# Kernel optimization log

Measured on AMD Instinct MI355X. Metric: run time of the kernel, lower is better.

The kernel has to match this reference:

```python
import jax, jax.numpy as jnp
import numpy as np

B, D, N, MH, MV = 4, 1024, 2048, 1024, 1024

def setup_inputs() -> dict:
    key = jax.random.key(0)
    k1, k2, k3, k4, k5 = jax.random.split(key, 5)
    return {
        "x": jax.random.normal(k1, (B, D, N), dtype=jnp.float32),
        "W_Q": jax.random.normal(k2, (MH, D), dtype=jnp.float32),
        "W_K": jax.random.normal(k3, (MH, D), dtype=jnp.float32),
        "W_V": jax.random.normal(k4, (MV, D), dtype=jnp.float32),
        "W_O": jax.random.normal(k5, (D, MV), dtype=jnp.float32),
    }

def reference(x, W_Q, W_K, W_V, W_O):
    # x: [b, d, n] (feature-major). Projections: [b, m, n]
    q = jnp.einsum('hd,bdn->bhn', W_Q, x)
    k = jnp.einsum('hd,bdn->bhn', W_K, x)
    v = jnp.einsum('vd,bdn->bvn', W_V, x)
    # scores[b,i,j] = sum_h k[b,h,i] * q[b,h,j]  -> [b, n, n]; NOTE: no 1/sqrt scale (faithful)
    scores = jnp.einsum('bhi,bhj->bij', k, q)
    scores = jax.nn.softmax(scores, axis=-1)
    # v @ scores -> [b, m_V, n]
    attn = jnp.einsum('bvi,bij->bvj', v, scores)
    # W_O @ attn -> [b, d, n]
    return jnp.einsum('dv,bvj->bdj', W_O, attn)
```

## Files before the change

kernel.cpp:

```cpp
#include <hip/hip_runtime.h>
#include <cstddef>
#include <cstdint>

typedef unsigned short u16;
typedef __attribute__((ext_vector_type(8))) short bf16x8;
typedef __attribute__((ext_vector_type(8))) _Float16 f16x8;
typedef __attribute__((ext_vector_type(4))) float f32x4;
typedef __attribute__((ext_vector_type(16))) float f32x16;

#define GLOBAL_AS __attribute__((address_space(1)))
#define LDS_AS __attribute__((address_space(3)))

__device__ __forceinline__ void async16(const u16* g, u16* l) {
    __builtin_amdgcn_global_load_lds((GLOBAL_AS const uint32_t*)g,
                                     (LDS_AS uint32_t*)l, 16, 0, 0);
}

__device__ __forceinline__ u16 f2bf(float f) {
    uint32_t u = __builtin_bit_cast(uint32_t, f);
    uint32_t r = (u + 0x7FFFu + ((u >> 16) & 1u)) >> 16;
    return (u16)r;
}

__global__ __launch_bounds__(256)
void wprep(const float* __restrict__ WQ, const float* __restrict__ WK,
           const float* __restrict__ WV, const float* __restrict__ WO,
           u16* __restrict__ DQ, u16* __restrict__ DK,
           u16* __restrict__ DV, u16* __restrict__ DOb)
{
    const int role = blockIdx.z;
    __shared__ float t[32][33];
    int tx = threadIdx.x & 31, ty = threadIdx.x >> 5;
    int c0 = blockIdx.x * 32, r0 = blockIdx.y * 32;
    const float* S = role == 0 ? WQ : role == 1 ? WK : role == 2 ? WV : WO;

    if (role == 3) {
        #pragma unroll
        for (int k = 0; k < 4; ++k) {
            size_t o = (size_t)(r0 + ty + 8 * k) * 1024 + c0 + tx;
            DOb[o] = f2bf(S[o]);
        }
        return;
    }
    #pragma unroll
    for (int k = 0; k < 4; ++k)
        t[ty + 8 * k][tx] = S[(size_t)(r0 + ty + 8 * k) * 1024 + c0 + tx];
    __syncthreads();
    if (role == 2) {
        #pragma unroll
        for (int k = 0; k < 4; ++k)
            DV[(size_t)(c0 + ty + 8 * k) * 1024 + r0 + tx] = f2bf(t[tx][ty + 8 * k]);
    } else {
        u16* D = role == 0 ? DQ : DK;
        #pragma unroll
        for (int k = 0; k < 4; ++k) {
            float a = t[tx][ty + 8 * k] * 64.0f;
            _Float16 h0 = (_Float16)a;
            _Float16 h1 = (_Float16)(a - (float)h0);
            size_t o = (size_t)(c0 + ty + 8 * k) * 1024 + r0 + tx;
            D[o] = __builtin_bit_cast(u16, h0);
            D[1048576 + o] = __builtin_bit_cast(u16, h1);
        }
    }
}

__global__ __launch_bounds__(256)
void xprep(const float* __restrict__ Sb, size_t sBatch,
           u16* __restrict__ BFb, size_t bfBatch,
           u16* __restrict__ Db, size_t dBatch, size_t plane)
{
    const float* S = Sb + blockIdx.z * sBatch;
    u16* BF = BFb + blockIdx.z * bfBatch;
    u16* D = Db + blockIdx.z * dBatch;
    __shared__ float t[32][33];
    int tx = threadIdx.x & 31, ty = threadIdx.x >> 5;
    int c0 = blockIdx.x * 32, r0 = blockIdx.y * 32;
    #pragma unroll
    for (int k = 0; k < 4; ++k) {
        float v = S[(size_t)(r0 + ty + 8 * k) * 2048 + c0 + tx];
        t[ty + 8 * k][tx] = v;
        BF[(size_t)(r0 + ty + 8 * k) * 2048 + c0 + tx] = f2bf(v);
    }
    __syncthreads();
    #pragma unroll
    for (int k = 0; k < 4; ++k) {
        float a = t[tx][ty + 8 * k] * 64.0f;
        _Float16 h0 = (_Float16)a;
        _Float16 h1 = (_Float16)(a - (float)h0);
        size_t o = (size_t)(c0 + ty + 8 * k) * 1024 + r0 + tx;
        D[o] = __builtin_bit_cast(u16, h0);
        D[plane + o] = __builtin_bit_cast(u16, h1);
    }
}

__global__ __launch_bounds__(256)
void tbf16(const u16* __restrict__ Sb, size_t sBatch, u16* __restrict__ Db, size_t dBatch)
{
    const u16* S = Sb + blockIdx.z * sBatch;
    u16* D = Db + blockIdx.z * dBatch;
    __shared__ u16 t[32][34];
    int tx = threadIdx.x & 31, ty = threadIdx.x >> 5;
    int c0 = blockIdx.x * 32, r0 = blockIdx.y * 32;
    #pragma unroll
    for (int k = 0; k < 4; ++k)
        t[ty + 8 * k][tx] = S[(size_t)(r0 + ty + 8 * k) * 2048 + c0 + tx];
    __syncthreads();
    #pragma unroll
    for (int k = 0; k < 4; ++k)
        D[(size_t)(c0 + ty + 8 * k) * 2048 + r0 + tx] = t[tx][ty + 8 * k];
}

#define MMF4(AF, BF)                                                                   \
    _Pragma("unroll") for (int i = 0; i < 4; ++i)                                      \
        _Pragma("unroll") for (int j = 0; j < 4; ++j)                                  \
            acc[i][j] = __builtin_amdgcn_mfma_f32_16x16x32_f16(AF[i], BF[j], acc[i][j], 0, 0, 0);
#define MMB4(AF, BF)                                                                   \
    _Pragma("unroll") for (int i = 0; i < 4; ++i)                                      \
        _Pragma("unroll") for (int j = 0; j < 4; ++j)                                  \
            acc[i][j] = __builtin_amdgcn_mfma_f32_16x16x32_bf16(AF[i], BF[j], acc[i][j], 0, 0, 0);

template<int TERMS, int SPLITK>
__global__ __launch_bounds__(256)
void gemm_big(const u16* __restrict__ Ab, size_t aPlane,
              const u16* __restrict__ Bb, size_t bPlane,
              float* __restrict__ Cb, size_t cBatch,
              int M, int N, int K)
{
    constexpr int RSZ = 4096;
    constexpr int BUF = (TERMS == 3 ? 4 : 2) * RSZ;
    __shared__ u16 lds[2 * BUF];
    const u16* A = Ab;
    const u16* B = Bb;
    const int z = blockIdx.z;
    const int kt0 = SPLITK ? z * (K >> 2) : 0;
    const int kend = SPLITK ? kt0 + (K >> 2) : K;
    const int tid = threadIdx.x;
    const int lane = tid & 63, wave = tid >> 6;
    const int m0 = blockIdx.y * 128, n0 = blockIdx.x * 128;
    const int l15 = lane & 15, q = lane >> 4;
    const int rm = (wave >> 1) * 64, rn = (wave & 1) * 64;

    int sr[2], sg[2], sbase[2];
    #pragma unroll
    for (int it = 0; it < 2; ++it) {
        int s = tid + it * 256;
        sr[it] = s >> 2;
        sg[it] = (s & 3) ^ ((sr[it] >> 1) & 3);
        sbase[it] = (it * 256 + wave * 64) * 8;
    }
    const int fsw = (q ^ ((l15 >> 1) & 3)) * 8;
    int aoff[4], boff[4];
    #pragma unroll
    for (int f = 0; f < 4; ++f) {
        aoff[f] = (rm + f * 16 + l15) * 32 + fsw;
        boff[f] = (rn + f * 16 + l15) * 32 + fsw;
    }

    f32x4 acc[4][4];
    #pragma unroll
    for (int i = 0; i < 4; ++i)
        #pragma unroll
        for (int j = 0; j < 4; ++j)
            acc[i][j] = (f32x4){0.f, 0.f, 0.f, 0.f};

#define STAGEB(PP, KT)                                                                 \
    do {                                                                               \
        _Pragma("unroll")                                                              \
        for (int it = 0; it < 2; ++it) {                                               \
            const size_t ao = (size_t)(m0 + sr[it]) * K + (KT) + sg[it] * 8;           \
            const size_t bo = (size_t)(n0 + sr[it]) * K + (KT) + sg[it] * 8;           \
            const int d = (PP) * BUF + sbase[it];                                      \
            if (TERMS == 3) {                                                          \
                async16(A + ao, &lds[d]);                                              \
                async16(A + aPlane + ao, &lds[d + RSZ]);                               \
                async16(B + bo, &lds[d + 2 * RSZ]);                                    \
                async16(B + bPlane + bo, &lds[d + 3 * RSZ]);                           \
            } else {                                                                   \
                async16(A + ao, &lds[d]);                                              \
                async16(B + bo, &lds[d + RSZ]);                                        \
            }                                                                          \
        }                                                                              \
    } while (0)

    STAGEB(0, kt0);
    for (int kt = kt0; kt < kend; kt += 32) {
        const int p = (kt >> 5) & 1;
        __syncthreads();
        if (kt + 32 < kend) STAGEB(p ^ 1, kt + 32);
        const u16* L = &lds[p * BUF];
        if (TERMS == 3) {
            f16x8 a0f[4], b0f[4], xf[4];
            #pragma unroll
            for (int f = 0; f < 4; ++f) a0f[f] = *(const f16x8*)&L[aoff[f]];
            #pragma unroll
            for (int f = 0; f < 4; ++f) b0f[f] = *(const f16x8*)&L[2 * RSZ + boff[f]];
            MMF4(a0f, b0f);
            #pragma unroll
            for (int f = 0; f < 4; ++f) xf[f] = *(const f16x8*)&L[3 * RSZ + boff[f]];
            MMF4(a0f, xf);
            #pragma unroll
            for (int f = 0; f < 4; ++f) xf[f] = *(const f16x8*)&L[RSZ + aoff[f]];
            MMF4(xf, b0f);
        } else {
            bf16x8 af[4], bf_[4];
            #pragma unroll
            for (int f = 0; f < 4; ++f) af[f] = *(const bf16x8*)&L[aoff[f]];
            #pragma unroll
            for (int f = 0; f < 4; ++f) bf_[f] = *(const bf16x8*)&L[RSZ + boff[f]];
            MMB4(af, bf_);
        }
    }
#undef STAGEB

    float* C = Cb + (size_t)z * cBatch;
    #pragma unroll
    for (int i = 0; i < 4; ++i) {
        int row = m0 + rm + i * 16 + q * 4;
        #pragma unroll
        for (int j = 0; j < 4; ++j) {
            int col = n0 + rn + j * 16 + l15;
            #pragma unroll
            for (int r = 0; r < 4; ++r)
                C[(size_t)(row + r) * N + col] = acc[i][j][r];
        }
    }
}

template<int EPI>
__global__ __launch_bounds__(256)
void reduce4(const float4* __restrict__ P, u16* __restrict__ D, size_t plane)
{
    size_t i = blockIdx.x * 256 + threadIdx.x;
    float4 a = P[i], b = P[262144 + i], c = P[524288 + i], d = P[786432 + i];
    float v[4] = { a.x + b.x + c.x + d.x, a.y + b.y + c.y + d.y,
                   a.z + b.z + c.z + d.z, a.w + b.w + c.w + d.w };
    if (EPI == 1) {
        #pragma unroll
        for (int k = 0; k < 4; ++k) {
            float vs = v[k] * 0.000244140625f;
            _Float16 h0 = (_Float16)vs;
            _Float16 h1 = (_Float16)(vs - (float)h0);
            D[i * 4 + k] = __builtin_bit_cast(u16, h0);
            D[plane + i * 4 + k] = __builtin_bit_cast(u16, h1);
        }
    } else {
        ushort4 o = { f2bf(v[0]), f2bf(v[1]), f2bf(v[2]), f2bf(v[3]) };
        *(ushort4*)&D[i * 4] = o;
    }
}

#define RDAF(dst, PL, H)                                                               \
    _Pragma("unroll")                                                                  \
    for (int f = 0; f < FM; ++f)                                                       \
        dst[f] = *(const f16x8*)&L[(PL) * ASZ + arow[f] * 32 + ((2 * (H) + half) ^ asw[f]) * 8];
#define RDBF(dst, PL, H)                                                               \
    _Pragma("unroll")                                                                  \
    for (int f = 0; f < FN; ++f)                                                       \
        dst[f] = *(const f16x8*)&L[2 * ASZ + (PL) * BSZ + brow[f] * 32 + ((2 * (H) + half) ^ bsw[f]) * 8];
#define MMW(AF, BF)                                                                    \
    _Pragma("unroll")                                                                  \
    for (int i = 0; i < FM; ++i)                                                       \
        _Pragma("unroll")                                                              \
        for (int j = 0; j < FN; ++j)                                                   \
            acc[i][j] = __builtin_amdgcn_mfma_f32_32x32x16_f16(AF[i], BF[j], acc[i][j], 0, 0, 0);
#define MMWB(AF, BF)                                                                   \
    _Pragma("unroll")                                                                  \
    for (int i = 0; i < FM; ++i)                                                       \
        _Pragma("unroll")                                                              \
        for (int j = 0; j < FN; ++j)                                                   \
            acc[i][j] = __builtin_amdgcn_mfma_f32_32x32x16_bf16(AF[i], BF[j], acc[i][j], 0, 0, 0);

template<int TERMS, int EPI, int TM, int TN, int WGM, int WGN>
__global__ __launch_bounds__(512, 2)
void gemm_w(const u16* __restrict__ Ab, size_t aBatch, size_t aPlane,
            const u16* __restrict__ Bb, size_t bBatch, size_t bPlane,
            void* __restrict__ Cb, size_t cBatch, size_t cPlane,
            int M, int N, int K)
{
    constexpr int ASZ = TM * 32;
    constexpr int BSZ = TN * 32;
    constexpr int APL = (TERMS == 3) ? 2 : 1;
    constexpr int BUF = APL * (ASZ + BSZ);
    constexpr int FM = TM / WGM / 32;
    constexpr int FN = TN / WGN / 32;
    constexpr int AIT = TM / 128;
    constexpr int BIT = TN / 128;
    extern __shared__ __align__(16) u16 lds[];

    int bid = blockIdx.x + gridDim.x * blockIdx.y;
    int cpr = gridDim.x >> 2;
    int c8 = bid & 7, kk = bid >> 3;
    int bx = (kk % cpr) * 4 + (c8 & 3);
    int by = (kk / cpr) * 2 + (c8 >> 2);

    const u16* A = Ab + blockIdx.z * aBatch;
    const u16* B = Bb + blockIdx.z * bBatch;
    const int tid = threadIdx.x;
    const int lane = tid & 63, wave = tid >> 6;
    const int m0 = by * TM, n0 = bx * TN;
    const int l31 = lane & 31, half = lane >> 5;
    const int rm = (wave / WGN) * (TM / WGM);
    const int rn = (wave % WGN) * (TN / WGN);

    int arow[FM], asw[FM], brow[FN], bsw[FN];
    #pragma unroll
    for (int f = 0; f < FM; ++f) { arow[f] = rm + f * 32 + l31; asw[f] = (arow[f] >> 1) & 3; }
    #pragma unroll
    for (int f = 0; f < FN; ++f) { brow[f] = rn + f * 32 + l31; bsw[f] = (brow[f] >> 1) & 3; }

    f32x16 acc[FM][FN];
    #pragma unroll
    for (int i = 0; i < FM; ++i)
        #pragma unroll
        for (int j = 0; j < FN; ++j)
            #pragma unroll
            for (int r = 0; r < 16; ++r) acc[i][j][r] = 0.f;

    auto stage = [&](int pp, int kt) {
        #pragma unroll
        for (int it = 0; it < AIT; ++it) {
            int s = tid + it * 512;
            int r = s >> 2;
            int g = (s & 3) ^ ((r >> 1) & 3);
            int base = pp * BUF + (it * 512 + wave * 64) * 8;
            size_t go = (size_t)(m0 + r) * K + kt + g * 8;
            async16(A + go, &lds[base]);
            if (TERMS == 3) async16(A + aPlane + go, &lds[base + ASZ]);
        }
        #pragma unroll
        for (int it = 0; it < BIT; ++it) {
            int s = tid + it * 512;
            int r = s >> 2;
            int g = (s & 3) ^ ((r >> 1) & 3);
            int base = pp * BUF + APL * ASZ + (it * 512 + wave * 64) * 8;
            size_t go = (size_t)(n0 + r) * K + kt + g * 8;
            async16(B + go, &lds[base]);
            if (TERMS == 3) async16(B + bPlane + go, &lds[base + BSZ]);
        }
    };

    stage(0, 0);
    for (int kt = 0; kt < K; kt += 32) {
        const int p = (kt >> 5) & 1;
        __syncthreads();
        if (kt + 32 < K) stage(p ^ 1, kt + 32);
        const u16* L = &lds[p * BUF];
        if (TERMS == 3) {
            f16x8 A0h0[FM], A0h1[FM], B0h0[FN], B0h1[FN];
            f16x8 B1h0[FN], B1h1[FN], A1h0[FM], A1h1[FM];
            RDAF(A0h0, 0, 0) RDBF(B0h0, 0, 0)
            RDAF(A0h1, 0, 1) RDBF(B0h1, 0, 1)
            RDBF(B1h0, 1, 0)
            MMW(A0h0, B0h0)
            RDBF(B1h1, 1, 1)
            MMW(A0h1, B0h1)
            RDAF(A1h0, 1, 0)
            MMW(A0h0, B1h0)
            MMW(A0h1, B1h1)
            RDAF(A1h1, 1, 1)
            MMW(A1h0, B0h0)
            MMW(A1h1, B0h1)
        } else {
            bf16x8 Ah0[FM], Ah1[FM], Bh0[FN], Bh1[FN];
            #pragma unroll
            for (int f = 0; f < FM; ++f)
                Ah0[f] = *(const bf16x8*)&L[arow[f] * 32 + (half ^ asw[f]) * 8];
            #pragma unroll
            for (int f = 0; f < FN; ++f)
                Bh0[f] = *(const bf16x8*)&L[ASZ + brow[f] * 32 + (half ^ bsw[f]) * 8];
            #pragma unroll
            for (int f = 0; f < FM; ++f)
                Ah1[f] = *(const bf16x8*)&L[arow[f] * 32 + ((2 + half) ^ asw[f]) * 8];
            #pragma unroll
            for (int f = 0; f < FN; ++f)
                Bh1[f] = *(const bf16x8*)&L[ASZ + brow[f] * 32 + ((2 + half) ^ bsw[f]) * 8];
            MMWB(Ah0, Bh0)
            MMWB(Ah1, Bh1)
        }
    }

    #pragma unroll
    for (int i = 0; i < FM; ++i) {
        #pragma unroll
        for (int j = 0; j < FN; ++j) {
            int col = n0 + rn + j * 32 + l31;
            #pragma unroll
            for (int r = 0; r < 16; ++r) {
                int row = m0 + rm + i * 32 + (r & 3) + 8 * (r >> 2) + 4 * half;
                float v = acc[i][j][r];
                size_t o = (size_t)row * N + col;
                if (EPI == 0) {
                    ((float*)Cb + blockIdx.z * cBatch)[o] = v;
                } else if (EPI == 1) {
                    u16* C0 = (u16*)Cb + blockIdx.z * cBatch;
                    float vs = v * 0.000244140625f;
                    _Float16 h0 = (_Float16)vs;
                    _Float16 h1 = (_Float16)(vs - (float)h0);
                    C0[o] = __builtin_bit_cast(u16, h0);
                    C0[cPlane + o] = __builtin_bit_cast(u16, h1);
                } else {
                    ((u16*)Cb + blockIdx.z * cBatch)[o] = f2bf(v);
                }
            }
        }
    }
}

#undef RDAF
#undef RDBF
#undef MMW
#undef MMWB

__global__ __launch_bounds__(256)
void softmax_p(const float* __restrict__ Sb, size_t sBatch, u16* __restrict__ Pb, size_t pBatch)
{
    const float* S = Sb + blockIdx.y * sBatch + (size_t)blockIdx.x * 2048;
    u16* P = Pb + blockIdx.y * pBatch + (size_t)blockIdx.x * 2048;
    const int tid = threadIdx.x;

    float4 v0 = *(const float4*)&S[tid * 4];
    float4 v1 = *(const float4*)&S[1024 + tid * 4];

    float m = fmaxf(fmaxf(fmaxf(v0.x, v0.y), fmaxf(v0.z, v0.w)),
                    fmaxf(fmaxf(v1.x, v1.y), fmaxf(v1.z, v1.w)));
    #pragma unroll
    for (int off = 32; off > 0; off >>= 1)
        m = fmaxf(m, __shfl_xor(m, off, 64));
    __shared__ float redm[4];
    if ((tid & 63) == 0) redm[tid >> 6] = m;
    __syncthreads();
    m = fmaxf(fmaxf(redm[0], redm[1]), fmaxf(redm[2], redm[3]));

    v0.x = __expf(v0.x - m); v0.y = __expf(v0.y - m);
    v0.z = __expf(v0.z - m); v0.w = __expf(v0.w - m);
    v1.x = __expf(v1.x - m); v1.y = __expf(v1.y - m);
    v1.z = __expf(v1.z - m); v1.w = __expf(v1.w - m);

    float s = v0.x + v0.y + v0.z + v0.w + v1.x + v1.y + v1.z + v1.w;
    #pragma unroll
    for (int off = 32; off > 0; off >>= 1)
        s += __shfl_xor(s, off, 64);
    __shared__ float reds[4];
    if ((tid & 63) == 0) reds[tid >> 6] = s;
    __syncthreads();
    s = reds[0] + reds[1] + reds[2] + reds[3];

    const float r = 1.0f / s;
    ushort4 o0 = { f2bf(v0.x * r), f2bf(v0.y * r), f2bf(v0.z * r), f2bf(v0.w * r) };
    ushort4 o1 = { f2bf(v1.x * r), f2bf(v1.y * r), f2bf(v1.z * r), f2bf(v1.w * r) };
    *(ushort4*)&P[tid * 4] = o0;
    *(ushort4*)&P[1024 + tid * 4] = o1;
}

extern "C" void kernel_launch(void* const* d_in, const int* in_sizes, int n_in,
                              void* d_out, int out_size, void* d_ws, size_t ws_size,
                              hipStream_t stream)
{
    const size_t MB = 1048576;
    const size_t WREG = 34 * MB;
    const size_t PER  = 32 * MB;
    const size_t PER_US = PER / 2, PER_F = PER / 4;

    char* ws = (char*)d_ws;
    u16* WQT2 = (u16*)ws;
    u16* WKT2 = (u16*)(ws + 4 * MB);
    u16* M2   = (u16*)(ws + 8 * MB);
    u16* WObf = (u16*)(ws + 12 * MB);
    u16* WVT  = (u16*)(ws + 14 * MB);
    u16* WOV  = (u16*)(ws + 16 * MB);
    u16* xbf  = (u16*)(ws + 18 * MB);

    int G = (ws_size >= WREG + 4 * PER) ? 4 : (ws_size >= WREG + 2 * PER) ? 2 : 1;

    const float* x = (const float*)d_in[0];
    float* out = (float*)d_out;
    dim3 blk(256);

    hipFuncSetAttribute((const void*)gemm_w<3, 0, 256, 256, 2, 4>,
                        hipFuncAttributeMaxDynamicSharedMemorySize, 131072);
    hipFuncSetAttribute((const void*)gemm_w<3, 1, 256, 128, 4, 2>,
                        hipFuncAttributeMaxDynamicSharedMemorySize, 98304);

    float* PART = (float*)(ws + WREG);
    wprep<<<dim3(32, 32, 4), blk, 0, stream>>>(
        (const float*)d_in[1], (const float*)d_in[2],
        (const float*)d_in[3], (const float*)d_in[4],
        WQT2, WKT2, WVT, WObf);
    gemm_big<3, 1><<<dim3(8, 8, 4), blk, 0, stream>>>(WKT2, 1048576, WQT2, 1048576,
                                                      PART, 1048576, 1024, 1024, 1024);
    reduce4<1><<<1024, blk, 0, stream>>>((const float4*)PART, M2, 1048576);
    gemm_big<1, 1><<<dim3(8, 8, 4), blk, 0, stream>>>(WObf, 0, WVT, 0,
                                                      PART, 1048576, 1024, 1024, 1024);
    reduce4<2><<<1024, blk, 0, stream>>>((const float4*)PART, WOV, 0);

    for (int b0 = 0; b0 < 4; b0 += G) {
        char* R = ws + WREG;
        u16*   xT2 = (u16*)R;
        u16*   TT2 = (u16*)(R + 8 * MB);
        float* S32 = (float*)(R + 16 * MB);
        u16*   Pb  = (u16*)R;
        u16*   PTb = (u16*)(R + 8 * MB);
        u16*   XPT = (u16*)(R + 16 * MB);

        xprep<<<dim3(64, 32, G), blk, 0, stream>>>(x + (size_t)b0 * 2097152, 2097152,
                                                   xbf + (size_t)b0 * 2097152, 2097152,
                                                   xT2, PER_US, 2097152);
        gemm_w<3, 1, 256, 128, 4, 2><<<dim3(8, 8, G), 512, 98304, stream>>>(
            xT2, PER_US, 2097152, M2, 0, 1048576, TT2, PER_US, 2097152, 2048, 1024, 1024);
        gemm_w<3, 0, 256, 256, 2, 4><<<dim3(8, 8, G), 512, 131072, stream>>>(
            xT2, PER_US, 2097152, TT2, PER_US, 2097152, S32, PER_F, 0, 2048, 2048, 1024);
        softmax_p<<<dim3(2048, G), blk, 0, stream>>>(S32, PER_F, Pb, PER_US);
        tbf16<<<dim3(64, 64, G), blk, 0, stream>>>(Pb, PER_US, PTb, PER_US);
        gemm_w<1, 2, 256, 128, 4, 2><<<dim3(8, 8, G), 512, 49152, stream>>>(
            PTb, PER_US, 0, xbf + (size_t)b0 * 2097152, 2097152, 0,
            XPT, PER_US, 0, 2048, 1024, 2048);
        gemm_w<1, 0, 256, 128, 4, 2><<<dim3(16, 4, G), 512, 49152, stream>>>(
            WOV, 0, 0, XPT, PER_US, 0, out + (size_t)b0 * 2097152, 2097152, 0,
            1024, 2048, 1024);
    }
}
```

Baseline: 393.5 us.

## Fuse softmax with transpose and merge the two split-K reductions

Replaces the row-wise softmax kernel plus a separate bf16 transpose kernel with one kernel. Each block handles 32 score rows: it computes the row max and sum, then re-reads the scores through an LDS tile and writes the normalized probabilities already transposed. This removes the intermediate P buffer write and read and one launch per batch group. The two reduce4 launches for the weight-product partial sums are also merged into a single two-row grid. The trade-off is that the fused kernel reads the fp32 scores three times and runs far fewer blocks, so occupancy and latency hiding may suffer.

```diff
diff --git a/kernel.cpp b/kernel.cpp
--- a/kernel.cpp
+++ b/kernel.cpp
@@ -91,23 +91,6 @@
         D[o] = __builtin_bit_cast(u16, h0);
         D[plane + o] = __builtin_bit_cast(u16, h1);
     }
-}
-
-__global__ __launch_bounds__(256)
-void tbf16(const u16* __restrict__ Sb, size_t sBatch, u16* __restrict__ Db, size_t dBatch)
-{
-    const u16* S = Sb + blockIdx.z * sBatch;
-    u16* D = Db + blockIdx.z * dBatch;
-    __shared__ u16 t[32][34];
-    int tx = threadIdx.x & 31, ty = threadIdx.x >> 5;
-    int c0 = blockIdx.x * 32, r0 = blockIdx.y * 32;
-    #pragma unroll
-    for (int k = 0; k < 4; ++k)
-        t[ty + 8 * k][tx] = S[(size_t)(r0 + ty + 8 * k) * 2048 + c0 + tx];
-    __syncthreads();
-    #pragma unroll
-    for (int k = 0; k < 4; ++k)
-        D[(size_t)(c0 + ty + 8 * k) * 2048 + r0 + tx] = t[tx][ty + 8 * k];
 }
 
 #define MMF4(AF, BF)                                                                   \
@@ -226,26 +209,27 @@
     }
 }
 
-template<int EPI>
 __global__ __launch_bounds__(256)
-void reduce4(const float4* __restrict__ P, u16* __restrict__ D, size_t plane)
+void reduce4b(const float4* __restrict__ P1, const float4* __restrict__ P2,
+              u16* __restrict__ M2, u16* __restrict__ WOV)
 {
     size_t i = blockIdx.x * 256 + threadIdx.x;
+    const float4* P = blockIdx.y == 0 ? P1 : P2;
     float4 a = P[i], b = P[262144 + i], c = P[524288 + i], d = P[786432 + i];
     float v[4] = { a.x + b.x + c.x + d.x, a.y + b.y + c.y + d.y,
                    a.z + b.z + c.z + d.z, a.w + b.w + c.w + d.w };
-    if (EPI == 1) {
+    if (blockIdx.y == 0) {
         #pragma unroll
         for (int k = 0; k < 4; ++k) {
             float vs = v[k] * 0.000244140625f;
             _Float16 h0 = (_Float16)vs;
             _Float16 h1 = (_Float16)(vs - (float)h0);
-            D[i * 4 + k] = __builtin_bit_cast(u16, h0);
-            D[plane + i * 4 + k] = __builtin_bit_cast(u16, h1);
+            M2[i * 4 + k] = __builtin_bit_cast(u16, h0);
+            M2[1048576 + i * 4 + k] = __builtin_bit_cast(u16, h1);
         }
     } else {
         ushort4 o = { f2bf(v[0]), f2bf(v[1]), f2bf(v[2]), f2bf(v[3]) };
-        *(ushort4*)&D[i * 4] = o;
+        *(ushort4*)&WOV[i * 4] = o;
     }
 }
 
@@ -412,44 +396,50 @@
 #undef MMWB
 
 __global__ __launch_bounds__(256)
-void softmax_p(const float* __restrict__ Sb, size_t sBatch, u16* __restrict__ Pb, size_t pBatch)
-{
-    const float* S = Sb + blockIdx.y * sBatch + (size_t)blockIdx.x * 2048;
-    u16* P = Pb + blockIdx.y * pBatch + (size_t)blockIdx.x * 2048;
+void softmax_pt(const float* __restrict__ Sb, size_t sBatch,
+                u16* __restrict__ PTb, size_t pBatch)
+{
+    const float* S = Sb + blockIdx.y * sBatch + (size_t)blockIdx.x * 32 * 2048;
+    u16* PT = PTb + blockIdx.y * pBatch;
+    const int i0 = blockIdx.x * 32;
     const int tid = threadIdx.x;
-
-    float4 v0 = *(const float4*)&S[tid * 4];
-    float4 v1 = *(const float4*)&S[1024 + tid * 4];
-
-    float m = fmaxf(fmaxf(fmaxf(v0.x, v0.y), fmaxf(v0.z, v0.w)),
-                    fmaxf(fmaxf(v1.x, v1.y), fmaxf(v1.z, v1.w)));
-    #pragma unroll
-    for (int off = 32; off > 0; off >>= 1)
-        m = fmaxf(m, __shfl_xor(m, off, 64));
-    __shared__ float redm[4];
-    if ((tid & 63) == 0) redm[tid >> 6] = m;
-    __syncthreads();
-    m = fmaxf(fmaxf(redm[0], redm[1]), fmaxf(redm[2], redm[3]));
-
-    v0.x = __expf(v0.x - m); v0.y = __expf(v0.y - m);
-    v0.z = __expf(v0.z - m); v0.w = __expf(v0.w - m);
-    v1.x = __expf(v1.x - m); v1.y = __expf(v1.y - m);
-    v1.z = __expf(v1.z - m); v1.w = __expf(v1.w - m);
-
-    float s = v0.x + v0.y + v0.z + v0.w + v1.x + v1.y + v1.z + v1.w;
-    #pragma unroll
-    for (int off = 32; off > 0; off >>= 1)
-        s += __shfl_xor(s, off, 64);
-    __shared__ float reds[4];
-    if ((tid & 63) == 0) reds[tid >> 6] = s;
-    __syncthreads();
-    s = reds[0] + reds[1] + reds[2] + reds[3];
-
-    const float r = 1.0f / s;
-    ushort4 o0 = { f2bf(v0.x * r), f2bf(v0.y * r), f2bf(v0.z * r), f2bf(v0.w * r) };
-    ushort4 o1 = { f2bf(v1.x * r), f2bf(v1.y * r), f2bf(v1.z * r), f2bf(v1.w * r) };
-    *(ushort4*)&P[tid * 4] = o0;
-    *(ushort4*)&P[1024 + tid * 4] = o1;
+    const int row = tid >> 3, t8 = tid & 7;
+    __shared__ float mrow[32], rrow[32];
+    __shared__ float tbuf[32][33];
+
+    const float* Sr = S + (size_t)row * 2048;
+    float m = -3.4e38f;
+    for (int c = 0; c < 64; ++c) {
+        float4 x = *(const float4*)&Sr[(t8 + c * 8) * 4];
+        m = fmaxf(m, fmaxf(fmaxf(x.x, x.y), fmaxf(x.z, x.w)));
+    }
+    #pragma unroll
+    for (int off = 1; off < 8; off <<= 1)
+        m = fmaxf(m, __shfl_xor(m, off, 8));
+    float s = 0.f;
+    for (int c = 0; c < 64; ++c) {
+        float4 x = *(const float4*)&Sr[(t8 + c * 8) * 4];
+        s += __expf(x.x - m) + __expf(x.y - m) + __expf(x.z - m) + __expf(x.w - m);
+    }
+    #pragma unroll
+    for (int off = 1; off < 8; off <<= 1)
+        s += __shfl_xor(s, off, 8);
+    if (t8 == 0) { mrow[row] = m; rrow[row] = 1.0f / s; }
+
+    int tx = tid & 31, ty = tid >> 5;
+    for (int j0 = 0; j0 < 2048; j0 += 32) {
+        __syncthreads();
+        #pragma unroll
+        for (int k = 0; k < 4; ++k)
+            tbuf[ty + 8 * k][tx] = S[(size_t)(ty + 8 * k) * 2048 + j0 + tx];
+        __syncthreads();
+        float mm = mrow[tx], rr = rrow[tx];
+        #pragma unroll
+        for (int k = 0; k < 4; ++k) {
+            float e = __expf(tbuf[tx][ty + 8 * k] - mm) * rr;
+            PT[(size_t)(j0 + ty + 8 * k) * 2048 + i0 + tx] = f2bf(e);
+        }
+    }
 }
 
 extern "C" void kernel_launch(void* const* d_in, const int* in_sizes, int n_in,
@@ -481,26 +471,26 @@
     hipFuncSetAttribute((const void*)gemm_w<3, 1, 256, 128, 4, 2>,
                         hipFuncAttributeMaxDynamicSharedMemorySize, 98304);
 
-    float* PART = (float*)(ws + WREG);
+    float* PART1 = (float*)(ws + WREG);
+    float* PART2 = (float*)(ws + WREG + 16 * MB);
     wprep<<<dim3(32, 32, 4), blk, 0, stream>>>(
         (const float*)d_in[1], (const float*)d_in[2],
         (const float*)d_in[3], (const float*)d_in[4],
         WQT2, WKT2, WVT, WObf);
     gemm_big<3, 1><<<dim3(8, 8, 4), blk, 0, stream>>>(WKT2, 1048576, WQT2, 1048576,
-                                                      PART, 1048576, 1024, 1024, 1024);
-    reduce4<1><<<1024, blk, 0, stream>>>((const float4*)PART, M2, 1048576);
+                                                      PART1, 1048576, 1024, 1024, 1024);
     gemm_big<1, 1><<<dim3(8, 8, 4), blk, 0, stream>>>(WObf, 0, WVT, 0,
-                                                      PART, 1048576, 1024, 1024, 1024);
-    reduce4<2><<<1024, blk, 0, stream>>>((const float4*)PART, WOV, 0);
+                                                      PART2, 1048576, 1024, 1024, 1024);
+    reduce4b<<<dim3(1024, 2), blk, 0, stream>>>((const float4*)PART1, (const float4*)PART2,
+                                                M2, WOV);
 
     for (int b0 = 0; b0 < 4; b0 += G) {
         char* R = ws + WREG;
         u16*   xT2 = (u16*)R;
         u16*   TT2 = (u16*)(R + 8 * MB);
         float* S32 = (float*)(R + 16 * MB);
-        u16*   Pb  = (u16*)R;
         u16*   PTb = (u16*)(R + 8 * MB);
-        u16*   XPT = (u16*)(R + 16 * MB);
+        u16*   XPT = (u16*)R;
 
         xprep<<<dim3(64, 32, G), blk, 0, stream>>>(x + (size_t)b0 * 2097152, 2097152,
                                                    xbf + (size_t)b0 * 2097152, 2097152,
@@ -509,8 +499,7 @@
             xT2, PER_US, 2097152, M2, 0, 1048576, TT2, PER_US, 2097152, 2048, 1024, 1024);
         gemm_w<3, 0, 256, 256, 2, 4><<<dim3(8, 8, G), 512, 131072, stream>>>(
             xT2, PER_US, 2097152, TT2, PER_US, 2097152, S32, PER_F, 0, 2048, 2048, 1024);
-        softmax_p<<<dim3(2048, G), blk, 0, stream>>>(S32, PER_F, Pb, PER_US);
-        tbf16<<<dim3(64, 64, G), blk, 0, stream>>>(Pb, PER_US, PTb, PER_US);
+        softmax_pt<<<dim3(64, G), blk, 0, stream>>>(S32, PER_F, PTb, PER_US);
         gemm_w<1, 2, 256, 128, 4, 2><<<dim3(8, 8, G), 512, 49152, stream>>>(
             PTb, PER_US, 0, xbf + (size_t)b0 * 2097152, 2097152, 0,
             XPT, PER_US, 0, 2048, 1024, 2048);
```

After: 418.2 us. 1.06x slower.
